# Performance work log

Hardware: AMD Instinct MI355X
Metric: run time of the kernel (lower is better)

Reference implementation:

```python
import jax, jax.numpy as jnp
import numpy as np
from jax import lax

B, C, OUT, H, W = 8, 512, 512, 64, 64
BN_EPS = 1e-5


def setup_inputs() -> dict:
    key = jax.random.key(0)
    ks = jax.random.split(key, 20)
    s = 1.0 / np.sqrt(C)
    d = {
        "input1": jax.random.normal(ks[0], (B, C, H, W), jnp.float32),
        "input2": jax.random.normal(ks[1], (B, C, H, W), jnp.float32),
        "wq1": jax.random.normal(ks[2], (C, C), jnp.float32) * s,
        "bq1": jnp.zeros((C,), jnp.float32),
        "wk1": jax.random.normal(ks[3], (C, C), jnp.float32) * s,
        "bk1": jnp.zeros((C,), jnp.float32),
        "wv1": jax.random.normal(ks[4], (C, C), jnp.float32) * s,
        "bv1": jnp.zeros((C,), jnp.float32),
        "wq2": jax.random.normal(ks[5], (C, C), jnp.float32) * s,
        "bq2": jnp.zeros((C,), jnp.float32),
        "wk2": jax.random.normal(ks[6], (C, C), jnp.float32) * s,
        "bk2": jnp.zeros((C,), jnp.float32),
        "wv2": jax.random.normal(ks[7], (C, C), jnp.float32) * s,
        "bv2": jnp.zeros((C,), jnp.float32),
        "w_lin": jax.random.normal(ks[8], (1, C), jnp.float32) * s,  # shared gate conv, no bias
        "w_cat": jax.random.normal(ks[9], (OUT, 2 * C, 3, 3), jnp.float32) * (1.0 / np.sqrt(2 * C * 9)),
        "bn_gamma": jnp.ones((OUT,), jnp.float32),
        "bn_beta": jnp.zeros((OUT,), jnp.float32),
    }
    return d


def _conv1x1(x, w, b):
    # x: [B,C,H,W], w: [O,C] -> [B,O,H,W]
    return jnp.einsum('bchw,oc->bohw', x, w) + b[None, :, None, None]


def _branch(x_q_src, x_kv_src, wq, bq, wk, bk, wv, bv, w_lin, x_resid):
    # matches: attn = softmax(k(x_kv) @ q(x_q)^T); out = attn^T @ v(x_kv)
    b, c, h, w = x_kv_src.shape
    n = h * w
    q = _conv1x1(x_q_src, wq, bq).reshape(b, c, n)      # [B,C,N] (from the OTHER input)
    k = _conv1x1(x_kv_src, wk, bk).reshape(b, c, n)
    v = _conv1x1(x_kv_src, wv, bv).reshape(b, c, n)
    attn = jnp.einsum('bkn,bcn->bkc', k, q)             # [B,C,C]
    attn = jax.nn.softmax(attn, axis=-1)
    out = jnp.einsum('bkc,bkn->bcn', attn, v).reshape(b, c, h, w)
    # sigmoid gate: linear(avgpool(x_resid)) -> scalar per batch
    pooled = jnp.mean(x_resid, axis=(2, 3))             # [B,C]
    a = jax.nn.sigmoid(pooled @ w_lin.T)                # [B,1]
    return out * a[:, :, None, None] + x_resid


def reference(input1, input2, wq1, bq1, wk1, bk1, wv1, bv1,
              wq2, bq2, wk2, bk2, wv2, bv2, w_lin, w_cat, bn_gamma, bn_beta):
    # branch 1: k1 from input1, q2 from input2, v1 from input1, gate from input1
    out1 = _branch(input2, input1, wq2, bq2, wk1, bk1, wv1, bv1, w_lin, input1)
    # branch 2: k2 from input2, q1 from input1, v2 from input2, gate from input2
    out2 = _branch(input1, input2, wq1, bq1, wk2, bk2, wv2, bv2, w_lin, input2)
    x = jnp.concatenate([out1, out2], axis=1)           # [B,2C,H,W]
    y = lax.conv_general_dilated(x, w_cat, (1, 1), 'SAME',
                                 dimension_numbers=('NCHW', 'OIHW', 'NCHW'))
    # BatchNorm2d in training mode: batch statistics over (N,H,W)
    mean = jnp.mean(y, axis=(0, 2, 3), keepdims=True)
    var = jnp.var(y, axis=(0, 2, 3), keepdims=True)
    y = (y - mean) * lax.rsqrt(var + BN_EPS)
    y = y * bn_gamma[None, :, None, None] + bn_beta[None, :, None, None]
    return jax.nn.relu(y)
```

## Files before the change

### kernel.cpp

```cpp
#include <hip/hip_runtime.h>


typedef unsigned short u16;
typedef unsigned int u32;
typedef float f32x4 __attribute__((ext_vector_type(4)));
typedef short bf16x8 __attribute__((ext_vector_type(8)));

#define DEV __device__ __forceinline__

DEV u16 f2bf(float f) {
  u32 u = __float_as_uint(f);
  return (u16)((u + 0x7fffu + ((u >> 16) & 1u)) >> 16);
}
DEV float bf2f(u16 u) { return __uint_as_float(((u32)u) << 16); }

DEV void gload_lds16(const void* g, void* l) {
  __builtin_amdgcn_global_load_lds(
      (const __attribute__((address_space(1))) void*)g,
      (__attribute__((address_space(3))) void*)l, 16, 0, 0);
}

DEV void stage_tile(u16* L, const u16* src, int row0, long ld, int k0, int wid, int lane) {
  int rr = lane >> 2;
  int cc = (lane & 3) << 3;
#pragma unroll
  for (int j = 0; j < 2; ++j) {
    int chunk = j * 4 + wid;
    const u16* g = src + (long)(row0 + chunk * 16 + rr) * ld + (k0 + cc);
    gload_lds16(g, L + chunk * 512);
  }
}

DEV float waveRedSum(float v) {
#pragma unroll
  for (int o = 32; o > 0; o >>= 1) v += __shfl_xor(v, o);
  return v;
}

DEV float blockReduceSum256(float v) {
  __shared__ float r[4];
  v = waveRedSum(v);
  int tid = threadIdx.x;
  if ((tid & 63) == 0) r[tid >> 6] = v;
  __syncthreads();
  return r[0] + r[1] + r[2] + r[3];
}

__global__ __launch_bounds__(256) void gemm_gramK(const float* __restrict__ X1,
                                                  const float* __restrict__ X2,
                                                  float* __restrict__ parts)
{
  __shared__ __align__(16) u16 lds[4 * 4096];
  const int z = blockIdx.z;
  const int half = z >> 3, b = z & 7;
  const int m0 = blockIdx.x * 128, n0 = blockIdx.y * 128;
  const int tid = threadIdx.x, wid = tid >> 6, lane = tid & 63;
  const int wr = wid >> 1, wc = wid & 1;
  const int r16 = lane & 15, koff = (lane >> 4) << 3;
  const float* A = X1 + (long)b * 2097152 + half * 2048;
  const float* Bp = X2 + (long)b * 2097152 + half * 2048;
  const int sr = tid >> 3;
  const int sc = (tid & 7) * 4;

  f32x4 acc[4][4];
#pragma unroll
  for (int i = 0; i < 4; ++i)
#pragma unroll
    for (int j = 0; j < 4; ++j) acc[i][j] = (f32x4){0.f, 0.f, 0.f, 0.f};

  for (int k0 = 0; k0 < 2048; k0 += 32) {
    __syncthreads();
#pragma unroll
    for (int rr = 0; rr < 128; rr += 32) {
      float4 va = *(const float4*)&A[(long)(m0 + rr + sr) * 4096 + k0 + sc];
      float4 vb = *(const float4*)&Bp[(long)(n0 + rr + sr) * 4096 + k0 + sc];
      float fa[4] = {va.x, va.y, va.z, va.w};
      float fb[4] = {vb.x, vb.y, vb.z, vb.w};
      u32 pah0 = 0, pah1 = 0, pal0 = 0, pal1 = 0;
      u32 pbh0 = 0, pbh1 = 0, pbl0 = 0, pbl1 = 0;
#pragma unroll
      for (int e = 0; e < 2; ++e) {
        u16 h = f2bf(fa[e]);      pah0 |= ((u32)h) << (16 * e);
        u16 lo = f2bf(fa[e] - bf2f(h)); pal0 |= ((u32)lo) << (16 * e);
        h = f2bf(fa[e + 2]);      pah1 |= ((u32)h) << (16 * e);
        lo = f2bf(fa[e + 2] - bf2f(h)); pal1 |= ((u32)lo) << (16 * e);
        h = f2bf(fb[e]);          pbh0 |= ((u32)h) << (16 * e);
        lo = f2bf(fb[e] - bf2f(h)); pbl0 |= ((u32)lo) << (16 * e);
        h = f2bf(fb[e + 2]);      pbh1 |= ((u32)h) << (16 * e);
        lo = f2bf(fb[e + 2] - bf2f(h)); pbl1 |= ((u32)lo) << (16 * e);
      }
      int off = (rr + sr) * 32 + sc;
      *(uint2*)&lds[off]         = make_uint2(pah0, pah1);
      *(uint2*)&lds[4096 + off]  = make_uint2(pal0, pal1);
      *(uint2*)&lds[8192 + off]  = make_uint2(pbh0, pbh1);
      *(uint2*)&lds[12288 + off] = make_uint2(pbl0, pbl1);
    }
    __syncthreads();
    bf16x8 ah[4], al[4], bh[4], bl[4];
#pragma unroll
    for (int mi = 0; mi < 4; ++mi) {
      ah[mi] = *(const bf16x8*)&lds[(wr * 64 + mi * 16 + r16) * 32 + koff];
      al[mi] = *(const bf16x8*)&lds[4096 + (wr * 64 + mi * 16 + r16) * 32 + koff];
    }
#pragma unroll
    for (int nj = 0; nj < 4; ++nj) {
      bh[nj] = *(const bf16x8*)&lds[8192 + (wc * 64 + nj * 16 + r16) * 32 + koff];
      bl[nj] = *(const bf16x8*)&lds[12288 + (wc * 64 + nj * 16 + r16) * 32 + koff];
    }
#pragma unroll
    for (int mi = 0; mi < 4; ++mi)
#pragma unroll
      for (int nj = 0; nj < 4; ++nj) {
        acc[mi][nj] = __builtin_amdgcn_mfma_f32_16x16x32_bf16(ah[mi], bh[nj], acc[mi][nj], 0, 0, 0);
        acc[mi][nj] = __builtin_amdgcn_mfma_f32_16x16x32_bf16(ah[mi], bl[nj], acc[mi][nj], 0, 0, 0);
        acc[mi][nj] = __builtin_amdgcn_mfma_f32_16x16x32_bf16(al[mi], bh[nj], acc[mi][nj], 0, 0, 0);
      }
  }

  const int rq = lane >> 4;
  float* O = parts + (long)z * 262144;
#pragma unroll
  for (int mi = 0; mi < 4; ++mi)
#pragma unroll
    for (int nj = 0; nj < 4; ++nj)
#pragma unroll
      for (int i = 0; i < 4; ++i) {
        int row = m0 + wr * 64 + mi * 16 + rq * 4 + i;
        int col = n0 + wc * 64 + nj * 16 + r16;
        O[(long)row * 512 + col] = acc[mi][nj][i];
      }
}

__global__ __launch_bounds__(256) void k_gsplit(const float* __restrict__ parts,
                                                u16* __restrict__ Gh, u16* __restrict__ Gl)
{
  for (long i = (long)blockIdx.x * 256 + threadIdx.x; i < 2097152; i += (long)gridDim.x * 256) {
    float v = parts[i] + parts[i + 2097152];
    u16 h = f2bf(v);
    Gh[i] = h;
    Gl[i] = f2bf(v - bf2f(h));
  }
}

constexpr int EP_SPLIT = 0, EP_LOGITS = 1, EP_BF16 = 2, EP_XCAT = 3;

struct GArgs {
  const u16* Ah[2]; const u16* Al[2];
  const u16* Bh[2]; const u16* Bl[2];
  long Az[2], Bz[2];
  void* O0[2]; void* O1[2];
  const float* f0[2]; const float* f1[2];
  const float* f2[2]; const float* f3[2];
  const u16* rptr[2];
};

template <int EP, bool SPLIT3>
__global__ __launch_bounds__(256) void gemm_tn2(GArgs ga, int lda, int ldb, int K, long Oz)
{
  __shared__ __align__(16) u16 lds[(SPLIT3 ? 4 : 2) * 4096];
  const int z = blockIdx.z;
  const int br = z >> 3, b = z & 7;
  const u16* pAh = ga.Ah[br] + (long)b * ga.Az[br];
  const u16* pBh = ga.Bh[br] + (long)b * ga.Bz[br];
  const u16* pAl = SPLIT3 ? ga.Al[br] + (long)b * ga.Az[br] : nullptr;
  const u16* pBl = SPLIT3 ? ga.Bl[br] + (long)b * ga.Bz[br] : nullptr;
  const int m0 = blockIdx.x * 128, n0 = blockIdx.y * 128;
  const int tid = threadIdx.x, wid = tid >> 6, lane = tid & 63;
  const int wr = wid >> 1, wc = wid & 1;
  const int r16 = lane & 15, koff = (lane >> 4) << 3;

  f32x4 acc[4][4];
#pragma unroll
  for (int i = 0; i < 4; ++i)
#pragma unroll
    for (int j = 0; j < 4; ++j) acc[i][j] = (f32x4){0.f, 0.f, 0.f, 0.f};

  for (int k0 = 0; k0 < K; k0 += 32) {
    __syncthreads();
    stage_tile(lds, pAh, m0, lda, k0, wid, lane);
    stage_tile(lds + 4096, pBh, n0, ldb, k0, wid, lane);
    if constexpr (SPLIT3) {
      stage_tile(lds + 8192, pAl, m0, lda, k0, wid, lane);
      stage_tile(lds + 12288, pBl, n0, ldb, k0, wid, lane);
    }
    __syncthreads();
    bf16x8 af[4], bfh[4], af2[4], bf2_[4];
#pragma unroll
    for (int mi = 0; mi < 4; ++mi)
      af[mi] = *(const bf16x8*)&lds[(wr * 64 + mi * 16 + r16) * 32 + koff];
#pragma unroll
    for (int nj = 0; nj < 4; ++nj)
      bfh[nj] = *(const bf16x8*)&lds[4096 + (wc * 64 + nj * 16 + r16) * 32 + koff];
    if constexpr (SPLIT3) {
#pragma unroll
      for (int mi = 0; mi < 4; ++mi)
        af2[mi] = *(const bf16x8*)&lds[8192 + (wr * 64 + mi * 16 + r16) * 32 + koff];
#pragma unroll
      for (int nj = 0; nj < 4; ++nj)
        bf2_[nj] = *(const bf16x8*)&lds[12288 + (wc * 64 + nj * 16 + r16) * 32 + koff];
    }
#pragma unroll
    for (int mi = 0; mi < 4; ++mi)
#pragma unroll
      for (int nj = 0; nj < 4; ++nj) {
        acc[mi][nj] = __builtin_amdgcn_mfma_f32_16x16x32_bf16(af[mi], bfh[nj], acc[mi][nj], 0, 0, 0);
        if constexpr (SPLIT3) {
          acc[mi][nj] = __builtin_amdgcn_mfma_f32_16x16x32_bf16(af[mi], bf2_[nj], acc[mi][nj], 0, 0, 0);
          acc[mi][nj] = __builtin_amdgcn_mfma_f32_16x16x32_bf16(af2[mi], bfh[nj], acc[mi][nj], 0, 0, 0);
        }
      }
  }

  const int rq = lane >> 4;
  const long off = (long)z * Oz;
  float g = 0.f;
  if constexpr (EP == EP_XCAT) g = ga.f1[br][b];
#pragma unroll
  for (int mi = 0; mi < 4; ++mi)
#pragma unroll
    for (int nj = 0; nj < 4; ++nj)
#pragma unroll
      for (int i = 0; i < 4; ++i) {
        int row = m0 + wr * 64 + mi * 16 + rq * 4 + i;
        int col = n0 + wc * 64 + nj * 16 + r16;
        float v = acc[mi][nj][i];
        if constexpr (EP == EP_SPLIT) {
          long idx = off + (long)row * 512 + col;
          u16 h = f2bf(v);
          ((u16*)ga.O0[br])[idx] = h;
          ((u16*)ga.O1[br])[idx] = f2bf(v - bf2f(h));
        } else if constexpr (EP == EP_LOGITS) {
          v += ga.f0[br][row] * ga.f3[br][b * 512 + col] + ga.f1[br][col] * ga.f2[br][b * 512 + row];
          ((float*)ga.O0[br])[off + (long)row * 512 + col] = v;
        } else if constexpr (EP == EP_BF16) {
          ((u16*)ga.O0[br])[off + (long)row * 512 + col] = f2bf(v);
        } else {
          float val = (v + ga.f0[br][b * 512 + col]) * g +
                      bf2f(ga.rptr[br][(long)b * 2097152 + (long)row * 512 + col]);
          int yy = row >> 6, xx = row & 63;
          long oidx = ((long)(b * 66 + yy + 1) * 66 + (xx + 1)) * 512 + col;
          ((u16*)ga.O0[br])[oidx] = f2bf(val);
        }
      }
}

#define MF(a, b, c) __builtin_amdgcn_mfma_f32_16x16x32_bf16(a, b, c, 0, 0, 0)
#define SCHEDB() __builtin_amdgcn_sched_barrier(0)
#define BAR() __builtin_amdgcn_s_barrier()
#define STG_B(QB, i) gload_lds16(xb + sbo[i] + kko, &lds[(QB) + ldsB0 + (i) * 4096])
#define STG_A(QB, i) gload_lds16(Arow + (i) * 294912L + Aoff, &lds[(QB) + ldsA0 + (i) * 2048])

#define PH(j, S0, S1, VMA, VMB)                                                      \
  if (pf) { S0; S1; asm volatile("s_waitcnt vmcnt(" VMA ")" ::: "memory"); }         \
  else    { asm volatile("s_waitcnt vmcnt(" VMB ")" ::: "memory"); }                 \
  BAR(); SCHEDB();                                                                   \
  {                                                                                  \
    bf16x8 a00 = *(const bf16x8*)&lds[pBase + aRd + (2 * (j)) * 1024 + sxa0];        \
    bf16x8 a01 = *(const bf16x8*)&lds[pBase + aRd + (2 * (j)) * 1024 + sxa1];        \
    bf16x8 a10 = *(const bf16x8*)&lds[pBase + aRd + (2 * (j) + 1) * 1024 + sxa0];    \
    bf16x8 a11 = *(const bf16x8*)&lds[pBase + aRd + (2 * (j) + 1) * 1024 + sxa1];    \
    asm volatile("s_waitcnt lgkmcnt(0)" ::: "memory");                               \
    SCHEDB();                                                                        \
    __builtin_amdgcn_s_setprio(1);                                                   \
    _Pragma("unroll")                                                                \
    for (int fn = 0; fn < 4; ++fn) {                                                 \
      acc[2 * (j)][fn] = MF(a00, bq[fn][0], acc[2 * (j)][fn]);                       \
      acc[2 * (j)][fn] = MF(a01, bq[fn][1], acc[2 * (j)][fn]);                       \
      acc[2 * (j) + 1][fn] = MF(a10, bq[fn][0], acc[2 * (j) + 1][fn]);               \
      acc[2 * (j) + 1][fn] = MF(a11, bq[fn][1], acc[2 * (j) + 1][fn]);               \
    }                                                                                \
    __builtin_amdgcn_s_setprio(0);                                                   \
    SCHEDB(); BAR();                                                                 \
  }

__global__ __launch_bounds__(512, 2) void k_conv8(const u16* __restrict__ W,
                                                  const u16* __restrict__ xA,
                                                  const u16* __restrict__ xB,
                                                  float* __restrict__ y)
{
  __shared__ __align__(16) u16 lds[65536];
  const int cid = ((blockIdx.x & 7) << 5) + (blockIdx.x >> 3);
  const int mx = cid >> 7, bz = (cid >> 4) & 7, ny = cid & 15;
  const int m0 = mx * 256, n0 = ny * 256;
  const long zoff = (long)bz * 2230272;

  const int tid = threadIdx.x;
  const int w = tid >> 6, l = tid & 63;
  const int wr = w >> 2, wcn = w & 3, wl = w & 3;
  const int lr = l >> 3, l7 = l & 7, l15 = l & 15, l4 = l >> 4;
  const int ss8 = (l7 ^ lr) << 3;

  long sbo[4];
#pragma unroll
  for (int i = 0; i < 4; ++i) {
    int n = n0 + i * 64 + w * 8 + lr;
    sbo[i] = (long)((n >> 6) * 66 + (n & 63)) * 512;
  }
  const u16* Arow = W + (long)(m0 + wr * 128 + wl * 8 + lr) * 9216 + ss8;
  const int ldsA0 = wr * 8192 + wl * 512;
  const int ldsB0 = 16384 + w * 512;
  const int sxa0 = (l4 ^ l7) << 3;
  const int sxa1 = ((l4 | 4) ^ l7) << 3;
  const int aRd = wr * 8192 + l15 * 64;
  const int bRd = 16384 + wcn * 4096 + l15 * 64;

  f32x4 acc[8][4];
#pragma unroll
  for (int i = 0; i < 8; ++i)
#pragma unroll
    for (int j = 0; j < 4; ++j) acc[i][j] = (f32x4){0.f, 0.f, 0.f, 0.f};

  {
    const u16* xb = xA + zoff;
    const long kko = ss8;
    const long Aoff = 0;
    STG_B(0, 0); STG_B(0, 1); STG_B(0, 2); STG_B(0, 3);
    STG_A(0, 0); STG_A(0, 1); STG_A(0, 2); STG_A(0, 3);
  }

  for (int t = 0; t < 144; ++t) {
    const int pBase = (t & 1) << 15;
    const int qBase = pBase ^ 32768;
    const int tau = t + 1;
    const bool pf = tau < 144;
    const int tap = tau >> 4, cc = (tau & 15) << 6;
    const u16* xb = ((cc & 512) ? xB : xA) + zoff;
    const long kko = (long)((tap / 3) * 66 + (tap % 3)) * 512 + (cc & 511) + ss8;
    const long Aoff = (long)tau * 64;
    bf16x8 bq[4][2];

    if (pf) { STG_B(qBase, 0); STG_B(qBase, 1); asm volatile("s_waitcnt vmcnt(5)" ::: "memory"); }
    else    { asm volatile("s_waitcnt vmcnt(3)" ::: "memory"); }
    BAR(); SCHEDB();
#pragma unroll
    for (int fn = 0; fn < 4; ++fn) {
      bq[fn][0] = *(const bf16x8*)&lds[pBase + bRd + fn * 1024 + sxa0];
      bq[fn][1] = *(const bf16x8*)&lds[pBase + bRd + fn * 1024 + sxa1];
    }
    {
      bf16x8 a00 = *(const bf16x8*)&lds[pBase + aRd + 0 * 1024 + sxa0];
      bf16x8 a01 = *(const bf16x8*)&lds[pBase + aRd + 0 * 1024 + sxa1];
      bf16x8 a10 = *(const bf16x8*)&lds[pBase + aRd + 1 * 1024 + sxa0];
      bf16x8 a11 = *(const bf16x8*)&lds[pBase + aRd + 1 * 1024 + sxa1];
      asm volatile("s_waitcnt lgkmcnt(0)" ::: "memory");
      SCHEDB();
      __builtin_amdgcn_s_setprio(1);
#pragma unroll
      for (int fn = 0; fn < 4; ++fn) {
        acc[0][fn] = MF(a00, bq[fn][0], acc[0][fn]);
        acc[0][fn] = MF(a01, bq[fn][1], acc[0][fn]);
        acc[1][fn] = MF(a10, bq[fn][0], acc[1][fn]);
        acc[1][fn] = MF(a11, bq[fn][1], acc[1][fn]);
      }
      __builtin_amdgcn_s_setprio(0);
      SCHEDB(); BAR();
    }
    PH(1, STG_B(qBase, 2), STG_B(qBase, 3), "6", "2")
    PH(2, STG_A(qBase, 0), STG_A(qBase, 1), "7", "1")
    PH(3, STG_A(qBase, 2), STG_A(qBase, 3), "8", "0")
  }

#pragma unroll
  for (int fm = 0; fm < 8; ++fm)
#pragma unroll
    for (int fn = 0; fn < 4; ++fn)
#pragma unroll
      for (int i = 0; i < 4; ++i) {
        int row = m0 + wr * 128 + fm * 16 + l4 * 4 + i;
        int col = n0 + wcn * 64 + fn * 16 + l15;
        y[((long)bz * 512 + row) * 4096 + col] = acc[fm][fn][i];
      }
}

__global__ __launch_bounds__(256) void k_border(u16* __restrict__ xcat, float* __restrict__ rsum)
{
  const long base = (long)blockIdx.x * 2230272;
  const int tid = threadIdx.x;
  const uint4 z4 = make_uint4(0, 0, 0, 0);
  for (int i = tid; i < 8448; i += 256) {
    long off = (i < 4224) ? (long)i * 8 : (long)65 * 66 * 512 + (long)(i - 4224) * 8;
    *(uint4*)&xcat[base + off] = z4;
  }
  for (int i = tid; i < 8192; i += 256) {
    int y = 1 + (i >> 7);
    int xsel = (i >> 6) & 1;
    int v = i & 63;
    long off = ((long)y * 66 + (xsel ? 65 : 0)) * 512 + (long)v * 8;
    *(uint4*)&xcat[base + off] = z4;
  }
  if (blockIdx.x == 0) {
    float4 f4 = {0.f, 0.f, 0.f, 0.f};
    for (int i = tid; i < 2048; i += 256) ((float4*)rsum)[i] = f4;
  }
}

__global__ __launch_bounds__(256) void k_prep(const float* __restrict__ src,
                                              u16* __restrict__ xT, float* __restrict__ rsum)
{
  __shared__ float t[64][65];
  const int b = blockIdx.z, cb = blockIdx.y, nb = blockIdx.x;
  const float* s = src + (long)b * 2097152;
  const int tid = threadIdx.x;
#pragma unroll
  for (int it = 0; it < 4; ++it) {
    int cr = it * 16 + (tid >> 4);
    int nc = (tid & 15) * 4;
    float4 v = *(const float4*)&s[(long)(cb * 64 + cr) * 4096 + nb * 64 + nc];
    t[cr][nc] = v.x; t[cr][nc + 1] = v.y; t[cr][nc + 2] = v.z; t[cr][nc + 3] = v.w;
  }
  __syncthreads();
  int nr = tid >> 2, cs = (tid & 3) * 16;
  u16 hh[16] __attribute__((aligned(16)));
#pragma unroll
  for (int j = 0; j < 16; ++j) hh[j] = f2bf(t[cs + j][nr]);
  long d = (long)b * 2097152 + (long)(nb * 64 + nr) * 512 + cb * 64 + cs;
  *(uint4*)&xT[d] = *(const uint4*)&hh[0];
  *(uint4*)&xT[d + 8] = *(const uint4*)&hh[8];
  if (tid < 64) {
    float sum = 0.f;
#pragma unroll 8
    for (int j = 0; j < 64; ++j) sum += t[tid][j];
    atomicAdd(&rsum[b * 512 + cb * 64 + tid], sum);
  }
}

__global__ __launch_bounds__(256) void k_tr(const float* __restrict__ src, u16* __restrict__ dst,
                                            int scols, int srows, long zsrc, long zdst)
{
  __shared__ float t[64][65];
  src += (long)blockIdx.z * zsrc;
  dst += (long)blockIdx.z * zdst;
  const int c0 = blockIdx.x * 64, r0 = blockIdx.y * 64;
  const int tid = threadIdx.x;
#pragma unroll
  for (int it = 0; it < 4; ++it) {
    int rr = it * 16 + (tid >> 4);
    int cc = (tid & 15) * 4;
    float4 v = *(const float4*)&src[(long)(r0 + rr) * scols + c0 + cc];
    t[rr][cc] = v.x; t[rr][cc + 1] = v.y; t[rr][cc + 2] = v.z; t[rr][cc + 3] = v.w;
  }
  __syncthreads();
  int nr = tid >> 2, cs = (tid & 3) * 16;
  u16 hh[16] __attribute__((aligned(16)));
#pragma unroll
  for (int j = 0; j < 16; ++j) hh[j] = f2bf(t[cs + j][nr]);
  long d = (long)(c0 + nr) * srows + r0 + cs;
  *(uint4*)&dst[d] = *(const uint4*)&hh[0];
  *(uint4*)&dst[d + 8] = *(const uint4*)&hh[8];
}

__global__ __launch_bounds__(256) void k_gate(const float* __restrict__ rowsum,
                                              const float* __restrict__ wlin,
                                              float* __restrict__ gates)
{
  int id = blockIdx.x;
  int inp = id >> 3, b = id & 7;
  int tid = threadIdx.x;
  float s = 0.f;
  for (int c = tid; c < 512; c += 256) s += rowsum[inp * 4096 + b * 512 + c] * wlin[c];
  s = blockReduceSum256(s);
  if (tid == 0) gates[id] = 1.f / (1.f + __expf(-s / 4096.f));
}

__global__ __launch_bounds__(256) void k_skq(const float* __restrict__ wk1, const float* __restrict__ wq2,
                                             const float* __restrict__ wk2, const float* __restrict__ wq1,
                                             const float* __restrict__ bq2, const float* __restrict__ bq1,
                                             const float* __restrict__ rowsum, float* __restrict__ S)
{
  int which = blockIdx.y, b = blockIdx.z;
  int row = blockIdx.x * 4 + (threadIdx.x >> 6);
  int lane = threadIdx.x & 63;
  const float* W; const float* rs; const float* bias = nullptr;
  if (which == 0)      { W = wk1; rs = rowsum + b * 512; }
  else if (which == 1) { W = wq2; rs = rowsum + 4096 + b * 512; bias = bq2; }
  else if (which == 2) { W = wk2; rs = rowsum + 4096 + b * 512; }
  else                 { W = wq1; rs = rowsum + b * 512; bias = bq1; }
  float s = 0.f;
  for (int i = lane; i < 512; i += 64) s += W[row * 512 + i] * rs[i];
  s = waveRedSum(s);
  if (lane == 0) S[(which * 8 + b) * 512 + row] = s + (bias ? 4096.f * bias[row] : 0.f);
}

__global__ __launch_bounds__(256) void k_mbias(const u16* __restrict__ attnT,
                                               const float* __restrict__ bv1,
                                               const float* __restrict__ bv2,
                                               float* __restrict__ mb)
{
  int z = blockIdx.y;
  int c = blockIdx.x * 4 + (threadIdx.x >> 6);
  int lane = threadIdx.x & 63;
  const float* bv = (z >= 8) ? bv2 : bv1;
  const u16* row = attnT + (long)z * 262144 + (long)c * 512;
  float s = 0.f;
  for (int k = lane; k < 512; k += 64) s += bf2f(row[k]) * bv[k];
  s = waveRedSum(s);
  if (lane == 0) mb[z * 512 + c] = s;
}

struct SplitArgs { const float* s[4]; u16* h[4]; u16* l[4]; };
__global__ __launch_bounds__(256) void k_split4(SplitArgs a)
{
  int which = blockIdx.x >> 8;
  const float* s = a.s[which];
  u16* h = a.h[which];
  u16* l = a.l[which];
  for (int i = (blockIdx.x & 255) * 256 + threadIdx.x; i < 262144; i += 65536) {
    float v = s[i];
    u16 hh = f2bf(v);
    h[i] = hh;
    l[i] = f2bf(v - bf2f(hh));
  }
}
__global__ void k_wcat(const float* __restrict__ src, u16* __restrict__ dst) {
  const int n = 512 * 9 * 1024;
  for (int i = blockIdx.x * blockDim.x + threadIdx.x; i < n; i += gridDim.x * blockDim.x) {
    int ic = i & 1023;
    int r = i >> 10;
    int t = r % 9;
    int o = r / 9;
    dst[i] = f2bf(src[((long)o * 1024 + ic) * 9 + t]);
  }
}

__global__ __launch_bounds__(256) void k_softmaxT(const float* __restrict__ L,
                                                  u16* __restrict__ attnT)
{
  const int bid = blockIdx.x;
  const int z = bid >> 4, rg = bid & 15;
  const int w = threadIdx.x >> 6, lane = threadIdx.x & 63;
  const int a0 = rg * 32 + w * 8;
  const float* Lz = L + (long)z * 262144;
  u16* Az = attnT + (long)z * 262144;
  u32 pk[8][4] = {};
#pragma unroll
  for (int it = 0; it < 8; ++it) {
    long base = (long)(a0 + it) * 512 + lane * 8;
    float4 p0 = *(const float4*)&Lz[base], p1 = *(const float4*)&Lz[base + 4];
    float v[8] = {p0.x, p0.y, p0.z, p0.w, p1.x, p1.y, p1.z, p1.w};
    float m = v[0];
#pragma unroll
    for (int j = 1; j < 8; ++j) m = fmaxf(m, v[j]);
#pragma unroll
    for (int o = 32; o > 0; o >>= 1) m = fmaxf(m, __shfl_xor(m, o));
    float e[8], s = 0.f;
#pragma unroll
    for (int j = 0; j < 8; ++j) { e[j] = __expf(v[j] - m); s += e[j]; }
    s = waveRedSum(s);
    float inv = 1.f / s;
#pragma unroll
    for (int j = 0; j < 8; ++j)
      pk[j][it >> 1] |= ((u32)f2bf(e[j] * inv)) << ((it & 1) * 16);
  }
#pragma unroll
  for (int j = 0; j < 8; ++j) {
    int c = lane * 8 + j;
    *(uint4*)&Az[(long)c * 512 + a0] = make_uint4(pk[j][0], pk[j][1], pk[j][2], pk[j][3]);
  }
}

__global__ __launch_bounds__(256) void k_bnreduce(const float* __restrict__ y,
                                                  const float* __restrict__ gamma,
                                                  const float* __restrict__ beta,
                                                  float* __restrict__ sc, float* __restrict__ sh)
{
  int o = blockIdx.x, tid = threadIdx.x;
  float s = 0.f, s2 = 0.f;
  for (int b = 0; b < 8; ++b) {
    const float* p = y + ((long)b * 512 + o) * 4096;
    for (int i = tid * 4; i < 4096; i += 1024) {
      float4 v = *(const float4*)&p[i];
      s += v.x + v.y + v.z + v.w;
      s2 += v.x * v.x + v.y * v.y + v.z * v.z + v.w * v.w;
    }
  }
  s = waveRedSum(s);
  s2 = waveRedSum(s2);
  __shared__ float r[8];
  if ((tid & 63) == 0) { r[tid >> 6] = s; r[4 + (tid >> 6)] = s2; }
  __syncthreads();
  if (tid == 0) {
    float S = r[0] + r[1] + r[2] + r[3], S2 = r[4] + r[5] + r[6] + r[7];
    float mean = S / 32768.f;
    float var = S2 / 32768.f - mean * mean;
    float rstd = rsqrtf(var + 1e-5f);
    float scale = gamma[o] * rstd;
    sc[o] = scale;
    sh[o] = beta[o] - mean * scale;
  }
}

__global__ __launch_bounds__(256) void k_bnapply(float* __restrict__ y,
                                                 const float* __restrict__ sc,
                                                 const float* __restrict__ sh)
{
  const long n = 16777216;
  for (long i = ((long)blockIdx.x * 256 + threadIdx.x) * 4; i < n; i += (long)gridDim.x * 1024) {
    float4 v = *(const float4*)&y[i];
    int o = (int)((i >> 12) & 511);
    float a = sc[o], c = sh[o];
    v.x = fmaxf(v.x * a + c, 0.f);
    v.y = fmaxf(v.y * a + c, 0.f);
    v.z = fmaxf(v.z * a + c, 0.f);
    v.w = fmaxf(v.w * a + c, 0.f);
    *(float4*)&y[i] = v;
  }
}

extern "C" void kernel_launch(void* const* d_in, const int* in_sizes, int n_in,
                              void* d_out, int out_size, void* d_ws, size_t ws_size,
                              hipStream_t stream)
{
  (void)in_sizes; (void)n_in; (void)out_size; (void)ws_size;
  const float* in1 = (const float*)d_in[0];
  const float* in2 = (const float*)d_in[1];
  const float* wq1 = (const float*)d_in[2];  const float* bq1 = (const float*)d_in[3];
  const float* wk1 = (const float*)d_in[4];  const float* bk1 = (const float*)d_in[5];
  const float* wv1 = (const float*)d_in[6];  const float* bv1 = (const float*)d_in[7];
  const float* wq2 = (const float*)d_in[8];  const float* bq2 = (const float*)d_in[9];
  const float* wk2 = (const float*)d_in[10]; const float* bk2 = (const float*)d_in[11];
  const float* wv2 = (const float*)d_in[12]; const float* bv2 = (const float*)d_in[13];
  const float* wlin  = (const float*)d_in[14];
  const float* wcat  = (const float*)d_in[15];
  const float* gamma = (const float*)d_in[16];
  const float* beta  = (const float*)d_in[17];

  char* ws = (char*)d_ws;
  const size_t MB = 1024ull * 1024ull;
  u16* Gh     = (u16*)(ws + 0 * MB);
  u16* Gl     = (u16*)(ws + 4 * MB);
  u16* Mb     = (u16*)(ws + 0 * MB);
  u16* Uh     = (u16*)(ws + 8 * MB);
  u16* attnT  = (u16*)(ws + 8 * MB);
  u16* Ul     = (u16*)(ws + 16 * MB);
  float* logits = (float*)(ws + 24 * MB);
  float* parts  = logits;
  u16* xcatA  = (u16*)(ws + 40 * MB);
  u16* xcatB  = xcatA + 8L * 2230272;
  u16* wcp    = (u16*)(ws + 112 * MB);
  u16* wsp    = (u16*)(ws + 122 * MB);
  u16* WvT1   = (u16*)(ws + 126 * MB);
  u16* WvT2   = WvT1 + 262144;
  float* rowsum = (float*)(ws + 127 * MB);
  float* gates  = (float*)(ws + 127 * MB + 32 * 1024);
  float* S      = (float*)(ws + 127 * MB + 36 * 1024);
  float* mb     = (float*)(ws + 127 * MB + 100 * 1024);
  float* bnsc   = (float*)(ws + 127 * MB + 132 * 1024);
  float* bnsh   = bnsc + 512;

  u16* wq1h = wsp + 0 * 262144; u16* wq1l = wsp + 1 * 262144;
  u16* wq2h = wsp + 2 * 262144; u16* wq2l = wsp + 3 * 262144;
  u16* wk1h = wsp + 4 * 262144; u16* wk1l = wsp + 5 * 262144;
  u16* wk2h = wsp + 6 * 262144; u16* wk2l = wsp + 7 * 262144;

  u16* xT1 = (u16*)d_out;
  u16* xT2 = (u16*)d_out + 16777216;
  float* ybuf = (float*)d_out;

  k_border<<<16, 256, 0, stream>>>(xcatA, rowsum);
  k_prep<<<dim3(64, 8, 8), 256, 0, stream>>>(in1, xT1, rowsum);
  k_prep<<<dim3(64, 8, 8), 256, 0, stream>>>(in2, xT2, rowsum + 4096);
  k_tr<<<dim3(8, 8, 1), 256, 0, stream>>>(wv1, WvT1, 512, 512, 0L, 0L);
  k_tr<<<dim3(8, 8, 1), 256, 0, stream>>>(wv2, WvT2, 512, 512, 0L, 0L);
  {
    SplitArgs sa;
    sa.s[0] = wq1; sa.h[0] = wq1h; sa.l[0] = wq1l;
    sa.s[1] = wq2; sa.h[1] = wq2h; sa.l[1] = wq2l;
    sa.s[2] = wk1; sa.h[2] = wk1h; sa.l[2] = wk1l;
    sa.s[3] = wk2; sa.h[3] = wk2h; sa.l[3] = wk2l;
    k_split4<<<1024, 256, 0, stream>>>(sa);
  }
  k_wcat<<<4096, 256, 0, stream>>>(wcat, wcp);
  k_gate<<<16, 256, 0, stream>>>(rowsum, wlin, gates);
  k_skq<<<dim3(128, 4, 8), 256, 0, stream>>>(wk1, wq2, wk2, wq1, bq2, bq1, rowsum, S);

  gemm_gramK<<<dim3(4, 4, 16), 256, 0, stream>>>(in1, in2, parts);
  k_gsplit<<<2048, 256, 0, stream>>>(parts, Gh, Gl);

  {
    GArgs ga = {};
    ga.Ah[0] = wq2h; ga.Al[0] = wq2l; ga.Ah[1] = wk2h; ga.Al[1] = wk2l;
    ga.Az[0] = 0; ga.Az[1] = 0;
    ga.Bh[0] = Gh; ga.Bl[0] = Gl; ga.Bh[1] = Gh; ga.Bl[1] = Gl;
    ga.Bz[0] = 262144; ga.Bz[1] = 262144;
    ga.O0[0] = Uh; ga.O0[1] = Uh; ga.O1[0] = Ul; ga.O1[1] = Ul;
    gemm_tn2<EP_SPLIT, true><<<dim3(4, 4, 16), 256, 0, stream>>>(ga, 512, 512, 512, 262144);
  }
  {
    GArgs ga = {};
    ga.Ah[0] = wk1h; ga.Al[0] = wk1l; ga.Az[0] = 0;
    ga.Ah[1] = Uh + 2097152; ga.Al[1] = Ul + 2097152; ga.Az[1] = 262144;
    ga.Bh[0] = Uh; ga.Bl[0] = Ul; ga.Bz[0] = 262144;
    ga.Bh[1] = wq1h; ga.Bl[1] = wq1l; ga.Bz[1] = 0;
    ga.O0[0] = logits; ga.O0[1] = logits;
    ga.f0[0] = bk1; ga.f1[0] = bq2; ga.f2[0] = S;        ga.f3[0] = S + 4096;
    ga.f0[1] = bk2; ga.f1[1] = bq1; ga.f2[1] = S + 8192; ga.f3[1] = S + 12288;
    gemm_tn2<EP_LOGITS, true><<<dim3(4, 4, 16), 256, 0, stream>>>(ga, 512, 512, 512, 262144);
  }
  k_softmaxT<<<256, 256, 0, stream>>>(logits, attnT);
  k_mbias<<<dim3(128, 16), 256, 0, stream>>>(attnT, bv1, bv2, mb);
  {
    GArgs ga = {};
    ga.Ah[0] = attnT; ga.Ah[1] = attnT + 2097152;
    ga.Az[0] = 262144; ga.Az[1] = 262144;
    ga.Bh[0] = WvT1; ga.Bh[1] = WvT2; ga.Bz[0] = 0; ga.Bz[1] = 0;
    ga.O0[0] = Mb; ga.O0[1] = Mb;
    gemm_tn2<EP_BF16, false><<<dim3(4, 4, 16), 256, 0, stream>>>(ga, 512, 512, 512, 262144);
  }
  {
    GArgs ga = {};
    ga.Ah[0] = xT1; ga.Ah[1] = xT2; ga.Az[0] = 2097152; ga.Az[1] = 2097152;
    ga.Bh[0] = Mb; ga.Bh[1] = Mb + 2097152; ga.Bz[0] = 262144; ga.Bz[1] = 262144;
    ga.O0[0] = xcatA; ga.O0[1] = xcatB;
    ga.f0[0] = mb; ga.f0[1] = mb + 4096;
    ga.f1[0] = gates; ga.f1[1] = gates + 8;
    ga.rptr[0] = xT1; ga.rptr[1] = xT2;
    gemm_tn2<EP_XCAT, false><<<dim3(32, 4, 16), 256, 0, stream>>>(ga, 512, 512, 512, 0);
  }

  k_conv8<<<256, 512, 0, stream>>>(wcp, xcatA, xcatB, ybuf);
  k_bnreduce<<<512, 256, 0, stream>>>(ybuf, gamma, beta, bnsc, bnsh);
  k_bnapply<<<4096, 256, 0, stream>>>(ybuf, bnsc, bnsh);
}
```

Before: 693.3 us.

## Fuse BatchNorm statistics into conv epilogue and remap blocks for XCD locality

```diff
diff --git a/kernel.cpp b/kernel.cpp
--- a/kernel.cpp
+++ b/kernel.cpp
@@ -51,9 +51,11 @@
                                                   float* __restrict__ parts)
 {
   __shared__ __align__(16) u16 lds[4 * 4096];
-  const int z = blockIdx.z;
+  const int bid = blockIdx.x;
+  const int cid = ((bid & 7) << 5) + (bid >> 3);
+  const int z = cid >> 4, xy = cid & 15;
   const int half = z >> 3, b = z & 7;
-  const int m0 = blockIdx.x * 128, n0 = blockIdx.y * 128;
+  const int m0 = (xy & 3) * 128, n0 = (xy >> 2) * 128;
   const int tid = threadIdx.x, wid = tid >> 6, lane = tid & 63;
   const int wr = wid >> 1, wc = wid & 1;
   const int r16 = lane & 15, koff = (lane >> 4) << 3;
@@ -154,17 +156,25 @@
   const u16* rptr[2];
 };
 
-template <int EP, bool SPLIT3>
+template <int EP, bool SPLIT3, bool FLAT>
 __global__ __launch_bounds__(256) void gemm_tn2(GArgs ga, int lda, int ldb, int K, long Oz)
 {
   __shared__ __align__(16) u16 lds[(SPLIT3 ? 4 : 2) * 4096];
-  const int z = blockIdx.z;
+  int bx, by, z;
+  if constexpr (FLAT) {
+    const int cid = ((blockIdx.x & 7) << 8) + (blockIdx.x >> 3);
+    z = cid >> 7;
+    const int xy = cid & 127;
+    bx = xy >> 2; by = xy & 3;
+  } else {
+    bx = blockIdx.x; by = blockIdx.y; z = blockIdx.z;
+  }
   const int br = z >> 3, b = z & 7;
   const u16* pAh = ga.Ah[br] + (long)b * ga.Az[br];
   const u16* pBh = ga.Bh[br] + (long)b * ga.Bz[br];
   const u16* pAl = SPLIT3 ? ga.Al[br] + (long)b * ga.Az[br] : nullptr;
   const u16* pBl = SPLIT3 ? ga.Bl[br] + (long)b * ga.Bz[br] : nullptr;
-  const int m0 = blockIdx.x * 128, n0 = blockIdx.y * 128;
+  const int m0 = bx * 128, n0 = by * 128;
   const int tid = threadIdx.x, wid = tid >> 6, lane = tid & 63;
   const int wr = wid >> 1, wc = wid & 1;
   const int r16 = lane & 15, koff = (lane >> 4) << 3;
@@ -276,11 +286,13 @@
 __global__ __launch_bounds__(512, 2) void k_conv8(const u16* __restrict__ W,
                                                   const u16* __restrict__ xA,
                                                   const u16* __restrict__ xB,
-                                                  float* __restrict__ y)
+                                                  float* __restrict__ y,
+                                                  float* __restrict__ bnsum,
+                                                  float* __restrict__ bnsum2)
 {
   __shared__ __align__(16) u16 lds[65536];
   const int cid = ((blockIdx.x & 7) << 5) + (blockIdx.x >> 3);
-  const int mx = cid >> 7, bz = (cid >> 4) & 7, ny = cid & 15;
+  const int bz = cid >> 5, mx = (cid >> 4) & 1, ny = cid & 15;
   const int m0 = mx * 256, n0 = ny * 256;
   const long zoff = (long)bz * 2230272;
 
@@ -323,10 +335,12 @@
     const int qBase = pBase ^ 32768;
     const int tau = t + 1;
     const bool pf = tau < 144;
-    const int tap = tau >> 4, cc = (tau & 15) << 6;
-    const u16* xb = ((cc & 512) ? xB : xA) + zoff;
-    const long kko = (long)((tap / 3) * 66 + (tap % 3)) * 512 + (cc & 511) + ss8;
-    const long Aoff = (long)tau * 64;
+    const int ccc = tau / 9;
+    const int tap = tau - ccc * 9;
+    const int cch = ccc << 6;
+    const u16* xb = ((cch & 512) ? xB : xA) + zoff;
+    const long kko = (long)((tap / 3) * 66 + (tap % 3)) * 512 + (cch & 511) + ss8;
+    const long Aoff = (long)(tap << 10) + cch;
     bf16x8 bq[4][2];
 
     if (pf) { STG_B(qBase, 0); STG_B(qBase, 1); asm volatile("s_waitcnt vmcnt(5)" ::: "memory"); }
@@ -370,9 +384,36 @@
         int col = n0 + wcn * 64 + fn * 16 + l15;
         y[((long)bz * 512 + row) * 4096 + col] = acc[fm][fn][i];
       }
-}
-
-__global__ __launch_bounds__(256) void k_border(u16* __restrict__ xcat, float* __restrict__ rsum)
+
+  __syncthreads();
+  float* fl = (float*)lds;
+#pragma unroll
+  for (int fm = 0; fm < 8; ++fm)
+#pragma unroll
+    for (int i = 0; i < 4; ++i) {
+      float s = acc[fm][0][i] + acc[fm][1][i] + acc[fm][2][i] + acc[fm][3][i];
+      float s2 = acc[fm][0][i] * acc[fm][0][i] + acc[fm][1][i] * acc[fm][1][i] +
+                 acc[fm][2][i] * acc[fm][2][i] + acc[fm][3][i] * acc[fm][3][i];
+#pragma unroll
+      for (int m = 1; m < 16; m <<= 1) { s += __shfl_xor(s, m); s2 += __shfl_xor(s2, m); }
+      if (l15 == 0) {
+        int r = wr * 128 + fm * 16 + l4 * 4 + i;
+        fl[r * 4 + wcn] = s;
+        fl[1024 + r * 4 + wcn] = s2;
+      }
+    }
+  __syncthreads();
+  {
+    int r = tid & 255;
+    int which = tid >> 8;
+    const float* p = fl + which * 1024 + r * 4;
+    float v = p[0] + p[1] + p[2] + p[3];
+    atomicAdd((which ? bnsum2 : bnsum) + m0 + r, v);
+  }
+}
+
+__global__ __launch_bounds__(256) void k_border(u16* __restrict__ xcat, float* __restrict__ rsum,
+                                                float* __restrict__ bnsum)
 {
   const long base = (long)blockIdx.x * 2230272;
   const int tid = threadIdx.x;
@@ -388,9 +429,11 @@
     long off = ((long)y * 66 + (xsel ? 65 : 0)) * 512 + (long)v * 8;
     *(uint4*)&xcat[base + off] = z4;
   }
+  float4 f4 = {0.f, 0.f, 0.f, 0.f};
   if (blockIdx.x == 0) {
-    float4 f4 = {0.f, 0.f, 0.f, 0.f};
     for (int i = tid; i < 2048; i += 256) ((float4*)rsum)[i] = f4;
+  } else if (blockIdx.x == 1) {
+    for (int i = tid; i < 256; i += 256) ((float4*)bnsum)[i] = f4;
   }
 }
 
@@ -558,35 +601,19 @@
   }
 }
 
-__global__ __launch_bounds__(256) void k_bnreduce(const float* __restrict__ y,
-                                                  const float* __restrict__ gamma,
-                                                  const float* __restrict__ beta,
-                                                  float* __restrict__ sc, float* __restrict__ sh)
-{
-  int o = blockIdx.x, tid = threadIdx.x;
-  float s = 0.f, s2 = 0.f;
-  for (int b = 0; b < 8; ++b) {
-    const float* p = y + ((long)b * 512 + o) * 4096;
-    for (int i = tid * 4; i < 4096; i += 1024) {
-      float4 v = *(const float4*)&p[i];
-      s += v.x + v.y + v.z + v.w;
-      s2 += v.x * v.x + v.y * v.y + v.z * v.z + v.w * v.w;
-    }
-  }
-  s = waveRedSum(s);
-  s2 = waveRedSum(s2);
-  __shared__ float r[8];
-  if ((tid & 63) == 0) { r[tid >> 6] = s; r[4 + (tid >> 6)] = s2; }
-  __syncthreads();
-  if (tid == 0) {
-    float S = r[0] + r[1] + r[2] + r[3], S2 = r[4] + r[5] + r[6] + r[7];
-    float mean = S / 32768.f;
-    float var = S2 / 32768.f - mean * mean;
-    float rstd = rsqrtf(var + 1e-5f);
-    float scale = gamma[o] * rstd;
-    sc[o] = scale;
-    sh[o] = beta[o] - mean * scale;
-  }
+__global__ __launch_bounds__(512) void k_bnstat(const float* __restrict__ bnsum,
+                                                const float* __restrict__ bnsum2,
+                                                const float* __restrict__ gamma,
+                                                const float* __restrict__ beta,
+                                                float* __restrict__ sc, float* __restrict__ sh)
+{
+  int o = threadIdx.x;
+  float mean = bnsum[o] / 32768.f;
+  float var = bnsum2[o] / 32768.f - mean * mean;
+  float rstd = rsqrtf(var + 1e-5f);
+  float scale = gamma[o] * rstd;
+  sc[o] = scale;
+  sh[o] = beta[o] - mean * scale;
 }
 
 __global__ __launch_bounds__(256) void k_bnapply(float* __restrict__ y,
@@ -644,8 +671,10 @@
   float* gates  = (float*)(ws + 127 * MB + 32 * 1024);
   float* S      = (float*)(ws + 127 * MB + 36 * 1024);
   float* mb     = (float*)(ws + 127 * MB + 100 * 1024);
-  float* bnsc   = (float*)(ws + 127 * MB + 132 * 1024);
-  float* bnsh   = bnsc + 512;
+  float* bnsum  = (float*)(ws + 127 * MB + 132 * 1024);
+  float* bnsum2 = (float*)(ws + 127 * MB + 134 * 1024);
+  float* bnsc   = (float*)(ws + 127 * MB + 136 * 1024);
+  float* bnsh   = (float*)(ws + 127 * MB + 138 * 1024);
 
   u16* wq1h = wsp + 0 * 262144; u16* wq1l = wsp + 1 * 262144;
   u16* wq2h = wsp + 2 * 262144; u16* wq2l = wsp + 3 * 262144;
@@ -656,7 +685,7 @@
   u16* xT2 = (u16*)d_out + 16777216;
   float* ybuf = (float*)d_out;
 
-  k_border<<<16, 256, 0, stream>>>(xcatA, rowsum);
+  k_border<<<16, 256, 0, stream>>>(xcatA, rowsum, bnsum);
   k_prep<<<dim3(64, 8, 8), 256, 0, stream>>>(in1, xT1, rowsum);
   k_prep<<<dim3(64, 8, 8), 256, 0, stream>>>(in2, xT2, rowsum + 4096);
   k_tr<<<dim3(8, 8, 1), 256, 0, stream>>>(wv1, WvT1, 512, 512, 0L, 0L);
@@ -673,7 +702,7 @@
   k_gate<<<16, 256, 0, stream>>>(rowsum, wlin, gates);
   k_skq<<<dim3(128, 4, 8), 256, 0, stream>>>(wk1, wq2, wk2, wq1, bq2, bq1, rowsum, S);
 
-  gemm_gramK<<<dim3(4, 4, 16), 256, 0, stream>>>(in1, in2, parts);
+  gemm_gramK<<<256, 256, 0, stream>>>(in1, in2, parts);
   k_gsplit<<<2048, 256, 0, stream>>>(parts, Gh, Gl);
 
   {
@@ -683,7 +712,7 @@
     ga.Bh[0] = Gh; ga.Bl[0] = Gl; ga.Bh[1] = Gh; ga.Bl[1] = Gl;
     ga.Bz[0] = 262144; ga.Bz[1] = 262144;
     ga.O0[0] = Uh; ga.O0[1] = Uh; ga.O1[0] = Ul; ga.O1[1] = Ul;
-    gemm_tn2<EP_SPLIT, true><<<dim3(4, 4, 16), 256, 0, stream>>>(ga, 512, 512, 512, 262144);
+    gemm_tn2<EP_SPLIT, true, false><<<dim3(4, 4, 16), 256, 0, stream>>>(ga, 512, 512, 512, 262144);
   }
   {
     GArgs ga = {};
@@ -694,7 +723,7 @@
     ga.O0[0] = logits; ga.O0[1] = logits;
     ga.f0[0] = bk1; ga.f1[0] = bq2; ga.f2[0] = S;        ga.f3[0] = S + 4096;
     ga.f0[1] = bk2; ga.f1[1] = bq1; ga.f2[1] = S + 8192; ga.f3[1] = S + 12288;
-    gemm_tn2<EP_LOGITS, true><<<dim3(4, 4, 16), 256, 0, stream>>>(ga, 512, 512, 512, 262144);
+    gemm_tn2<EP_LOGITS, true, false><<<dim3(4, 4, 16), 256, 0, stream>>>(ga, 512, 512, 512, 262144);
   }
   k_softmaxT<<<256, 256, 0, stream>>>(logits, attnT);
   k_mbias<<<dim3(128, 16), 256, 0, stream>>>(attnT, bv1, bv2, mb);
@@ -704,7 +733,7 @@
     ga.Az[0] = 262144; ga.Az[1] = 262144;
     ga.Bh[0] = WvT1; ga.Bh[1] = WvT2; ga.Bz[0] = 0; ga.Bz[1] = 0;
     ga.O0[0] = Mb; ga.O0[1] = Mb;
-    gemm_tn2<EP_BF16, false><<<dim3(4, 4, 16), 256, 0, stream>>>(ga, 512, 512, 512, 262144);
+    gemm_tn2<EP_BF16, false, false><<<dim3(4, 4, 16), 256, 0, stream>>>(ga, 512, 512, 512, 262144);
   }
   {
     GArgs ga = {};
@@ -714,10 +743,10 @@
     ga.f0[0] = mb; ga.f0[1] = mb + 4096;
     ga.f1[0] = gates; ga.f1[1] = gates + 8;
     ga.rptr[0] = xT1; ga.rptr[1] = xT2;
-    gemm_tn2<EP_XCAT, false><<<dim3(32, 4, 16), 256, 0, stream>>>(ga, 512, 512, 512, 0);
-  }
-
-  k_conv8<<<256, 512, 0, stream>>>(wcp, xcatA, xcatB, ybuf);
-  k_bnreduce<<<512, 256, 0, stream>>>(ybuf, gamma, beta, bnsc, bnsh);
+    gemm_tn2<EP_XCAT, false, true><<<2048, 256, 0, stream>>>(ga, 512, 512, 512, 0);
+  }
+
+  k_conv8<<<256, 512, 0, stream>>>(wcp, xcatA, xcatB, ybuf, bnsum, bnsum2);
+  k_bnstat<<<1, 512, 0, stream>>>(bnsum, bnsum2, gamma, beta, bnsc, bnsh);
   k_bnapply<<<4096, 256, 0, stream>>>(ybuf, bnsc, bnsh);
 }
```

New measurement: 675.9 us. -2.5%, faster.
